# Kernel optimization log

Hardware: AMD Instinct MI355X
Metric: run time of the kernel (lower is better)

Reference implementation:

```python
import jax, jax.numpy as jnp
import numpy as np

N_FEATURES = 128
LENGTH = 10.0  # length_scale
N_NODES = 10000
N_EDGES = 200000


def mlp(x, W1, b1, W2, b2):
    # embedding.MLP(in, hidden, out): Linear -> SiLU -> Linear
    return jax.nn.silu(x @ W1 + b1) @ W2 + b2


def positional_encoding(dist, n_features, length):
    # sinusoidal encoding of scalar distances -> [E, n_features]
    ranks = jnp.arange(n_features // 2, dtype=dist.dtype)
    arg = dist[:, None] * ranks[None, :] * (np.pi / length)  # [E, F/2]
    return jnp.concatenate([jnp.sin(arg), jnp.cos(arg)], axis=-1)


def setup_inputs() -> dict:
    key = jax.random.key(0)
    N, E, F = N_NODES, N_EDGES, N_FEATURES
    ks = jax.random.split(key, 10)
    d = {}
    d["edge_index"] = jax.random.randint(ks[0], (2, E), 0, N)
    d["invariant_node_features"] = jax.random.normal(ks[1], (N, F), dtype=jnp.float32)
    d["equivariant_node_features"] = jax.random.normal(ks[2], (N, F, 3), dtype=jnp.float32)
    d["invariant_edge_features"] = jax.random.normal(ks[3], (E, F), dtype=jnp.float32)
    d["edge_dist"] = jax.random.uniform(ks[4], (E,), dtype=jnp.float32, minval=0.1, maxval=10.0)
    d["edge_dir"] = jax.random.normal(ks[5], (E, 3), dtype=jnp.float32)
    # phi: MLP(2F -> F -> 5F); w: MLP(F -> F -> 5F)
    d["phi_W1"] = jax.random.normal(ks[6], (2 * F, F), dtype=jnp.float32) / np.sqrt(2 * F)
    d["phi_b1"] = jnp.zeros((F,), jnp.float32)
    d["phi_W2"] = jax.random.normal(ks[7], (F, 5 * F), dtype=jnp.float32) / np.sqrt(F)
    d["phi_b2"] = jnp.zeros((5 * F,), jnp.float32)
    d["w_W1"] = jax.random.normal(ks[8], (F, F), dtype=jnp.float32) / np.sqrt(F)
    d["w_b1"] = jnp.zeros((F,), jnp.float32)
    d["w_W2"] = jax.random.normal(ks[9], (F, 5 * F), dtype=jnp.float32) / np.sqrt(F)
    d["w_b2"] = jnp.zeros((5 * F,), jnp.float32)
    return d


def reference(edge_index, invariant_node_features, equivariant_node_features,
              invariant_edge_features, edge_dist, edge_dir,
              phi_W1, phi_b1, phi_W2, phi_b2, w_W1, w_b1, w_W2, w_b2):
    F = N_FEATURES
    src, dst = edge_index[0], edge_index[1]
    # gather + concat edge features -> phi input [E, 2F]
    in_feat = jnp.concatenate([invariant_node_features[src], invariant_edge_features], axis=-1)
    pe = positional_encoding(edge_dist, F, LENGTH)  # [E, F]
    m = mlp(in_feat, phi_W1, phi_b1, phi_W2, phi_b2) * mlp(pe, w_W1, w_b1, w_W2, w_b2)  # [E, 5F]
    gates, cp_gates, scale_edge_dir, ds, de = jnp.split(m, 5, axis=-1)
    src_eq = equivariant_node_features[src]            # [E, F, 3]
    dst_eq = equivariant_node_features[dst]            # [E, F, 3]
    edir = edge_dir[:, None, :]                        # [E, 1, 3]
    # multiply_first_dim(w, x) == w[..., None] * x for [E,F] x [E,F,3]
    gated_features = gates[..., None] * src_eq
    scaled_edge_dir = scale_edge_dir[..., None] * edir
    cross = jnp.cross(jnp.broadcast_to(edir, dst_eq.shape), dst_eq)  # [E, F, 3]
    gated_cross = cp_gates[..., None] * cross
    dv = scaled_edge_dir + gated_features + gated_cross  # [E, F, 3]
    N = invariant_node_features.shape[0]
    dv = jax.ops.segment_sum(dv, dst, num_segments=N)   # [N, F, 3]
    ds = jax.ops.segment_sum(ds, dst, num_segments=N)   # [N, F]
    return (equivariant_node_features + dv,
            invariant_node_features + ds,
            invariant_edge_features + de)
```

## Files before the change

### kernel.cpp

```cpp
#include <hip/hip_runtime.h>
#include <math.h>

#define E_EDGES 200000
#define N_NODES 10000
#define FDIM    128

typedef __attribute__((ext_vector_type(8))) short  short8;
typedef __attribute__((ext_vector_type(4))) float  float4v;

#define WT1_OFF   0
#define WTW1_OFF  32768
#define WT2_OFF   49152
#define WTW2_OFF  131072
#define W_TOTAL   212992
#define CNT_BYTE  425984
#define CUR_BYTE  465984
#define PERM_BYTE 505984

#define EQ_OUT_SZ   (N_NODES * FDIM * 3)
#define INV_OUT_SZ  (N_NODES * FDIM)

__device__ __forceinline__ unsigned short f2bf(float x) {
    union { float f; unsigned u; } v; v.f = x;
    unsigned r = v.u + 0x7fffu + ((v.u >> 16) & 1u);
    return (unsigned short)(r >> 16);
}
__device__ __forceinline__ float bf2f(unsigned short h) {
    union { unsigned u; float f; } v; v.u = ((unsigned)h) << 16; return v.f;
}

__global__ void prep_fused(const float* __restrict__ phiW1,
                           const float* __restrict__ wW1,
                           const float* __restrict__ phiW2,
                           const float* __restrict__ wW2,
                           unsigned short* __restrict__ ws,
                           int* __restrict__ counts,
                           const float* __restrict__ eq,
                           const float* __restrict__ inv,
                           float* __restrict__ out) {
    int t = blockIdx.x * 256 + threadIdx.x;
    if (t < N_NODES) counts[t] = 0;
    if (t < W_TOTAL) {
        if (t < 32768) {
            int n = t >> 8, k = t & 255;
            ws[WT1_OFF + t] = f2bf(phiW1[k * 128 + n]);
        } else if (t < 49152) {
            int i = t - 32768; int n = i >> 7, k = i & 127;
            ws[WTW1_OFF + i] = f2bf(wW1[k * 128 + n]);
        } else if (t < 131072) {
            int i = t - 49152; int n = i >> 7, k = i & 127;
            ws[WT2_OFF + i] = f2bf(phiW2[k * 640 + n]);
        } else {
            int i = t - 131072; int n = i >> 7, k = i & 127;
            ws[WTW2_OFF + i] = f2bf(wW2[k * 640 + n]);
        }
    }
    if (t < EQ_OUT_SZ / 4) {
        ((float4v*)out)[t] = ((const float4v*)eq)[t];
    } else {
        int u = t - EQ_OUT_SZ / 4;
        ((float4v*)(out + EQ_OUT_SZ))[u] = ((const float4v*)inv)[u];
    }
}

__global__ void hist_kernel(const int* __restrict__ eidx, int* __restrict__ counts) {
    int e = blockIdx.x * 256 + threadIdx.x;
    if (e < E_EDGES) atomicAdd(&counts[eidx[E_EDGES + e]], 1);
}
__global__ __launch_bounds__(1024)
void scan_kernel(const int* __restrict__ counts, int* __restrict__ cursor) {
    __shared__ int sums[1024];
    const int t = threadIdx.x;
    const int base = t * 10;
    int local[10];
    int s = 0;
    #pragma unroll
    for (int j = 0; j < 10; ++j) {
        int b = base + j;
        int v = (b < N_NODES) ? counts[b] : 0;
        local[j] = s; s += v;
    }
    sums[t] = s;
    __syncthreads();
    for (int off = 1; off < 1024; off <<= 1) {
        int v = (t >= off) ? sums[t - off] : 0;
        __syncthreads();
        sums[t] += v;
        __syncthreads();
    }
    int pre = (t > 0) ? sums[t - 1] : 0;
    #pragma unroll
    for (int j = 0; j < 10; ++j) {
        int b = base + j;
        if (b < N_NODES) cursor[b] = pre + local[j];
    }
}
__global__ void scatter_kernel(const int* __restrict__ eidx,
                               int* __restrict__ cursor, int* __restrict__ perm) {
    int e = blockIdx.x * 256 + threadIdx.x;
    if (e < E_EDGES) {
        int d = eidx[E_EDGES + e];
        int pos = atomicAdd(&cursor[d], 1);
        perm[pos] = e;
    }
}

__global__ __launch_bounds__(256, 3)
void edge_kernel(const int*   __restrict__ eidx,
                 const float* __restrict__ node_inv,
                 const float* __restrict__ eqf,
                 const float* __restrict__ edge_inv,
                 const float* __restrict__ dist,
                 const float* __restrict__ dir,
                 const float* __restrict__ phi_b1,
                 const float* __restrict__ phi_b2,
                 const float* __restrict__ w_b1,
                 const float* __restrict__ w_b2,
                 const unsigned short* __restrict__ wsW,
                 const int* __restrict__ perm,
                 float* __restrict__ out) {
    __shared__ __align__(16) unsigned char smem_u[34816];
    __shared__ unsigned short A1b[32][136];
    __shared__ int   s_e[32], s_src[32], s_dst[32];
    __shared__ float s_dir[32][3];

    unsigned short (*A1a)[136] = (unsigned short (*)[136])smem_u;
    unsigned short (*A2)[136]  = (unsigned short (*)[136])(smem_u + 8704);
    unsigned short (*H1)[136]  = (unsigned short (*)[136])(smem_u + 17408);
    unsigned short (*H2)[136]  = (unsigned short (*)[136])(smem_u + 26112);
    float (*DVS)[65][4]        = (float (*)[65][4])smem_u;

    const int tid = threadIdx.x;
    const int p0  = blockIdx.x * 32;

    if (tid < 32) {
        int e = perm[p0 + tid];
        s_e[tid]   = e;
        s_src[tid] = eidx[e];
        s_dst[tid] = eidx[E_EDGES + e];
        s_dir[tid][0] = dir[e * 3 + 0];
        s_dir[tid][1] = dir[e * 3 + 1];
        s_dir[tid][2] = dir[e * 3 + 2];
    }
    __syncthreads();

    {
        const int i   = tid >> 3;
        const int seg = tid & 7;
        const int e   = s_e[i];
        const int k0  = seg * 32;
        const float* base = (k0 < 128)
            ? (node_inv + (size_t)s_src[i] * 128 + k0)
            : (edge_inv + (size_t)e * 128 + (k0 - 128));
        unsigned short* dst_ls = (k0 < 128) ? &A1a[i][k0] : &A1b[i][k0 - 128];
        #pragma unroll
        for (int j = 0; j < 4; ++j) {
            float4v v0 = *(const float4v*)(base + j * 8);
            float4v v1 = *(const float4v*)(base + j * 8 + 4);
            short8 sv;
            #pragma unroll
            for (int u = 0; u < 4; ++u) {
                sv[u]     = (short)f2bf(v0[u]);
                sv[u + 4] = (short)f2bf(v1[u]);
            }
            *(short8*)(dst_ls + j * 8) = sv;
        }
        const float d   = dist[e];
        const float cst = 3.14159265358979323846f / 10.0f;
        #pragma unroll
        for (int j = 0; j < 2; ++j) {
            short8 sv;
            #pragma unroll
            for (int u = 0; u < 8; ++u) {
                int f = seg * 16 + j * 8 + u;
                float val = (f < 64) ? __sinf(d * (float)f * cst)
                                     : __cosf(d * (float)(f - 64) * cst);
                sv[u] = (short)f2bf(val);
            }
            *(short8*)&A2[i][seg * 16 + j * 8] = sv;
        }
    }
    __syncthreads();

    const int wv   = tid >> 6;
    const int ln   = tid & 63;
    const int l16  = ln & 15;
    const int quad = ln >> 4;

    const unsigned short* Wt1  = wsW + WT1_OFF;
    const unsigned short* Wtw1 = wsW + WTW1_OFF;
    const unsigned short* Wt2  = wsW + WT2_OFF;
    const unsigned short* Wtw2 = wsW + WTW2_OFF;

    const float4v zero4 = {0.f, 0.f, 0.f, 0.f};

    float4v acc1[2][2], acc2[2][2];
    #pragma unroll
    for (int rt = 0; rt < 2; ++rt)
        #pragma unroll
        for (int ct = 0; ct < 2; ++ct) { acc1[rt][ct] = zero4; acc2[rt][ct] = zero4; }

    #pragma unroll
    for (int kk = 0; kk < 4; ++kk) {
        const int k = kk * 32 + quad * 8;
        short8 a0 = *(const short8*)&A1a[l16][k];
        short8 a1 = *(const short8*)&A1a[16 + l16][k];
        #pragma unroll
        for (int ct = 0; ct < 2; ++ct) {
            const int n = wv * 32 + ct * 16 + l16;
            short8 b = *(const short8*)&Wt1[n * 256 + k];
            acc1[0][ct] = __builtin_amdgcn_mfma_f32_16x16x32_bf16(a0, b, acc1[0][ct], 0, 0, 0);
            acc1[1][ct] = __builtin_amdgcn_mfma_f32_16x16x32_bf16(a1, b, acc1[1][ct], 0, 0, 0);
        }
    }
    #pragma unroll
    for (int kk = 0; kk < 4; ++kk) {
        const int k = kk * 32 + quad * 8;
        short8 a0 = *(const short8*)&A1b[l16][k];
        short8 a1 = *(const short8*)&A1b[16 + l16][k];
        #pragma unroll
        for (int ct = 0; ct < 2; ++ct) {
            const int n = wv * 32 + ct * 16 + l16;
            short8 b = *(const short8*)&Wt1[n * 256 + 128 + k];
            acc1[0][ct] = __builtin_amdgcn_mfma_f32_16x16x32_bf16(a0, b, acc1[0][ct], 0, 0, 0);
            acc1[1][ct] = __builtin_amdgcn_mfma_f32_16x16x32_bf16(a1, b, acc1[1][ct], 0, 0, 0);
        }
    }
    #pragma unroll
    for (int kk = 0; kk < 4; ++kk) {
        const int k = kk * 32 + quad * 8;
        short8 a0 = *(const short8*)&A2[l16][k];
        short8 a1 = *(const short8*)&A2[16 + l16][k];
        #pragma unroll
        for (int ct = 0; ct < 2; ++ct) {
            const int n = wv * 32 + ct * 16 + l16;
            short8 b = *(const short8*)&Wtw1[n * 128 + k];
            acc2[0][ct] = __builtin_amdgcn_mfma_f32_16x16x32_bf16(a0, b, acc2[0][ct], 0, 0, 0);
            acc2[1][ct] = __builtin_amdgcn_mfma_f32_16x16x32_bf16(a1, b, acc2[1][ct], 0, 0, 0);
        }
    }
    #pragma unroll
    for (int ct = 0; ct < 2; ++ct) {
        const int n = wv * 32 + ct * 16 + l16;
        const float b1v  = phi_b1[n];
        const float bw1v = w_b1[n];
        #pragma unroll
        for (int rt = 0; rt < 2; ++rt)
            #pragma unroll
            for (int r = 0; r < 4; ++r) {
                const int row = rt * 16 + quad * 4 + r;
                float x = acc1[rt][ct][r] + b1v;
                H1[row][n] = f2bf(x / (1.f + __expf(-x)));
                float y = acc2[rt][ct][r] + bw1v;
                H2[row][n] = f2bf(y / (1.f + __expf(-y)));
            }
    }
    __syncthreads();

    float* eq_out   = out;
    float* inv_out  = out + EQ_OUT_SZ;
    float* edge_out = out + EQ_OUT_SZ + INV_OUT_SZ;

    short8 ha[2][4], hb[2][4];
    #pragma unroll
    for (int rt = 0; rt < 2; ++rt)
        #pragma unroll
        for (int kk = 0; kk < 4; ++kk) {
            const int k = kk * 32 + quad * 8;
            ha[rt][kk] = *(const short8*)&H1[rt * 16 + l16][k];
            hb[rt][kk] = *(const short8*)&H2[rt * 16 + l16][k];
        }
    __syncthreads();

    const int red_f = tid >> 2;
    const int red_c = tid & 3;

    #pragma unroll
    for (int fc2 = 0; fc2 < 2; ++fc2) {
        float4v mv[2][5];
        #pragma unroll
        for (int g = 0; g < 5; ++g) {
            const int n = g * 128 + fc2 * 64 + wv * 16 + l16;
            float4v p1a = zero4, p1b = zero4, p2a = zero4, p2b = zero4;
            #pragma unroll
            for (int kk = 0; kk < 4; ++kk) {
                const int k = kk * 32 + quad * 8;
                short8 b1f = *(const short8*)&Wt2[n * 128 + k];
                short8 b2f = *(const short8*)&Wtw2[n * 128 + k];
                p1a = __builtin_amdgcn_mfma_f32_16x16x32_bf16(ha[0][kk], b1f, p1a, 0, 0, 0);
                p1b = __builtin_amdgcn_mfma_f32_16x16x32_bf16(ha[1][kk], b1f, p1b, 0, 0, 0);
                p2a = __builtin_amdgcn_mfma_f32_16x16x32_bf16(hb[0][kk], b2f, p2a, 0, 0, 0);
                p2b = __builtin_amdgcn_mfma_f32_16x16x32_bf16(hb[1][kk], b2f, p2b, 0, 0, 0);
            }
            const float b2v  = phi_b2[n];
            const float bw2v = w_b2[n];
            mv[0][g] = (p1a + b2v) * (p2a + bw2v);
            mv[1][g] = (p1b + b2v) * (p2b + bw2v);
        }
        {
            const int fl = wv * 16 + l16;
            const int fg = fc2 * 64 + fl;
            #pragma unroll
            for (int rt = 0; rt < 2; ++rt) {
                #pragma unroll
                for (int r = 0; r < 4; ++r) {
                    const int row = rt * 16 + quad * 4 + r;
                    const float gate = mv[rt][0][r];
                    const float cpg  = mv[rt][1][r];
                    const float sc   = mv[rt][2][r];
                    const float dsv  = mv[rt][3][r];
                    const float dev  = mv[rt][4][r];
                    const int sn = s_src[row], dn = s_dst[row], e = s_e[row];
                    const float ex = s_dir[row][0], ey = s_dir[row][1], ez = s_dir[row][2];
                    const float* se = eqf + ((size_t)sn * 128 + fg) * 3;
                    const float* dq = eqf + ((size_t)dn * 128 + fg) * 3;
                    const float sx = se[0], sy = se[1], sz = se[2];
                    const float dx = dq[0], dy = dq[1], dz = dq[2];
                    const float cx = ey * dz - ez * dy;
                    const float cy = ez * dx - ex * dz;
                    const float cz = ex * dy - ey * dx;
                    float4v v;
                    v[0] = sc * ex + gate * sx + cpg * cx;
                    v[1] = sc * ey + gate * sy + cpg * cy;
                    v[2] = sc * ez + gate * sz + cpg * cz;
                    v[3] = dsv;
                    *(float4v*)&DVS[row][fl] = v;
                    edge_out[(size_t)e * 128 + fg] = bf2f(A1b[row][fg]) + dev;
                }
            }
        }
        __syncthreads();
        {
            const int fgr = fc2 * 64 + red_f;
            float acc = 0.f;
            int prev = s_dst[0];
            #pragma unroll
            for (int r = 0; r < 32; ++r) {
                const int d = s_dst[r];
                const float v = DVS[r][red_f][red_c];
                if (d != prev) {
                    if (red_c < 3) atomicAdd(eq_out + ((size_t)prev * 128 + fgr) * 3 + red_c, acc);
                    else           atomicAdd(inv_out + (size_t)prev * 128 + fgr, acc);
                    acc = 0.f; prev = d;
                }
                acc += v;
            }
            if (red_c < 3) atomicAdd(eq_out + ((size_t)prev * 128 + fgr) * 3 + red_c, acc);
            else           atomicAdd(inv_out + (size_t)prev * 128 + fgr, acc);
        }
        __syncthreads();
    }
}

extern "C" void kernel_launch(void* const* d_in, const int* in_sizes, int n_in,
                              void* d_out, int out_size, void* d_ws, size_t ws_size,
                              hipStream_t stream) {
    const int*   eidx     = (const int*)d_in[0];
    const float* node_inv = (const float*)d_in[1];
    const float* eqf      = (const float*)d_in[2];
    const float* edge_inv = (const float*)d_in[3];
    const float* dist     = (const float*)d_in[4];
    const float* dir      = (const float*)d_in[5];
    const float* phi_W1   = (const float*)d_in[6];
    const float* phi_b1   = (const float*)d_in[7];
    const float* phi_W2   = (const float*)d_in[8];
    const float* phi_b2   = (const float*)d_in[9];
    const float* w_W1     = (const float*)d_in[10];
    const float* w_b1     = (const float*)d_in[11];
    const float* w_W2     = (const float*)d_in[12];
    const float* w_b2     = (const float*)d_in[13];
    float* out = (float*)d_out;
    unsigned short* wsW = (unsigned short*)d_ws;
    int* counts = (int*)((char*)d_ws + CNT_BYTE);
    int* cursor = (int*)((char*)d_ws + CUR_BYTE);
    int* perm   = (int*)((char*)d_ws + PERM_BYTE);

    prep_fused<<<(EQ_OUT_SZ + INV_OUT_SZ) / 4 / 256, 256, 0, stream>>>(
        phi_W1, w_W1, phi_W2, w_W2, wsW, counts, eqf, node_inv, out);
    hist_kernel<<<(E_EDGES + 255) / 256, 256, 0, stream>>>(eidx, counts);
    scan_kernel<<<1, 1024, 0, stream>>>(counts, cursor);
    scatter_kernel<<<(E_EDGES + 255) / 256, 256, 0, stream>>>(eidx, cursor, perm);
    edge_kernel<<<E_EDGES / 32, 256, 0, stream>>>(eidx, node_inv, eqf, edge_inv, dist, dir,
                                                  phi_b1, phi_b2, w_b1, w_b2, wsW, perm, out);
}
```

Before: 713.5 us.

## Compute positional encoding in registers, swizzle LDS tiles, raise occupancy, remap blocks per XCD

Removes the A2 LDS tile by computing the sinusoidal positional encoding directly into MFMA operand registers, and shrinks shared memory by replacing padded rows with an XOR-swizzled layout. Together these cut LDS per block enough that launch bounds can be raised from 3 to 4 blocks per CU. Block IDs are remapped so each XCD processes a contiguous range of sorted edges, which should improve L2 locality for destination atomics. The edge-feature bf16 values are loaded into registers before the DVS buffer overwrites that LDS region. In exchange, register pressure rises and the sin/cos work is duplicated across the waves.

```diff
diff --git a/kernel.cpp b/kernel.cpp
--- a/kernel.cpp
+++ b/kernel.cpp
@@ -27,6 +27,17 @@
 }
 __device__ __forceinline__ float bf2f(unsigned short h) {
     union { unsigned u; float f; } v; v.u = ((unsigned)h) << 16; return v.f;
+}
+
+__device__ __forceinline__ unsigned short* tile_ptr(unsigned short* base, int row, int col) {
+    unsigned off = (unsigned)(row * 256 + col * 2);
+    off ^= (unsigned)((row & 7) << 4);
+    return (unsigned short*)((char*)base + off);
+}
+__device__ __forceinline__ float* dvs_ptr(float* base, int row, int fl, int c) {
+    unsigned off = (unsigned)(row * 1024 + fl * 16 + c * 4);
+    off ^= (unsigned)((row & 7) << 4);
+    return (float*)((char*)base + off);
 }
 
 __global__ void prep_fused(const float* __restrict__ phiW1,
@@ -105,7 +116,7 @@
     }
 }
 
-__global__ __launch_bounds__(256, 3)
+__global__ __launch_bounds__(256, 4)
 void edge_kernel(const int*   __restrict__ eidx,
                  const float* __restrict__ node_inv,
                  const float* __restrict__ eqf,
@@ -119,19 +130,25 @@
                  const unsigned short* __restrict__ wsW,
                  const int* __restrict__ perm,
                  float* __restrict__ out) {
-    __shared__ __align__(16) unsigned char smem_u[34816];
-    __shared__ unsigned short A1b[32][136];
+    __shared__ __align__(16) unsigned char smem_u[32768];
     __shared__ int   s_e[32], s_src[32], s_dst[32];
     __shared__ float s_dir[32][3];
-
-    unsigned short (*A1a)[136] = (unsigned short (*)[136])smem_u;
-    unsigned short (*A2)[136]  = (unsigned short (*)[136])(smem_u + 8704);
-    unsigned short (*H1)[136]  = (unsigned short (*)[136])(smem_u + 17408);
-    unsigned short (*H2)[136]  = (unsigned short (*)[136])(smem_u + 26112);
-    float (*DVS)[65][4]        = (float (*)[65][4])smem_u;
+    __shared__ float s_dist[32];
+
+    unsigned short* A1a = (unsigned short*)smem_u;
+    unsigned short* A1b = (unsigned short*)(smem_u + 8192);
+    unsigned short* H1  = (unsigned short*)(smem_u + 16384);
+    unsigned short* H2  = (unsigned short*)(smem_u + 24576);
+    float*          DVSf = (float*)smem_u;
 
     const int tid = threadIdx.x;
-    const int p0  = blockIdx.x * 32;
+
+    const int NW = E_EDGES / 32;
+    const int q  = NW >> 3, r8 = NW & 7;
+    const int xcd = blockIdx.x & 7, idx = blockIdx.x >> 3;
+    const int swz_bid = (xcd < r8) ? (xcd * (q + 1) + idx)
+                                   : (r8 * (q + 1) + (xcd - r8) * q + idx);
+    const int p0 = swz_bid * 32;
 
     if (tid < 32) {
         int e = perm[p0 + tid];
@@ -141,18 +158,19 @@
         s_dir[tid][0] = dir[e * 3 + 0];
         s_dir[tid][1] = dir[e * 3 + 1];
         s_dir[tid][2] = dir[e * 3 + 2];
+        s_dist[tid]  = dist[e];
     }
     __syncthreads();
 
     {
         const int i   = tid >> 3;
         const int seg = tid & 7;
-        const int e   = s_e[i];
         const int k0  = seg * 32;
-        const float* base = (k0 < 128)
-            ? (node_inv + (size_t)s_src[i] * 128 + k0)
-            : (edge_inv + (size_t)e * 128 + (k0 - 128));
-        unsigned short* dst_ls = (k0 < 128) ? &A1a[i][k0] : &A1b[i][k0 - 128];
+        const float* base;
+        unsigned short* tb;
+        int c0;
+        if (k0 < 128) { base = node_inv + (size_t)s_src[i] * 128 + k0; tb = A1a; c0 = k0; }
+        else          { base = edge_inv + (size_t)s_e[i]  * 128 + (k0 - 128); tb = A1b; c0 = k0 - 128; }
         #pragma unroll
         for (int j = 0; j < 4; ++j) {
             float4v v0 = *(const float4v*)(base + j * 8);
@@ -163,21 +181,7 @@
                 sv[u]     = (short)f2bf(v0[u]);
                 sv[u + 4] = (short)f2bf(v1[u]);
             }
-            *(short8*)(dst_ls + j * 8) = sv;
-        }
-        const float d   = dist[e];
-        const float cst = 3.14159265358979323846f / 10.0f;
-        #pragma unroll
-        for (int j = 0; j < 2; ++j) {
-            short8 sv;
-            #pragma unroll
-            for (int u = 0; u < 8; ++u) {
-                int f = seg * 16 + j * 8 + u;
-                float val = (f < 64) ? __sinf(d * (float)f * cst)
-                                     : __cosf(d * (float)(f - 64) * cst);
-                sv[u] = (short)f2bf(val);
-            }
-            *(short8*)&A2[i][seg * 16 + j * 8] = sv;
+            *(short8*)tile_ptr(tb, i, c0 + j * 8) = sv;
         }
     }
     __syncthreads();
@@ -203,8 +207,8 @@
     #pragma unroll
     for (int kk = 0; kk < 4; ++kk) {
         const int k = kk * 32 + quad * 8;
-        short8 a0 = *(const short8*)&A1a[l16][k];
-        short8 a1 = *(const short8*)&A1a[16 + l16][k];
+        short8 a0 = *(const short8*)tile_ptr(A1a, l16, k);
+        short8 a1 = *(const short8*)tile_ptr(A1a, 16 + l16, k);
         #pragma unroll
         for (int ct = 0; ct < 2; ++ct) {
             const int n = wv * 32 + ct * 16 + l16;
@@ -216,8 +220,8 @@
     #pragma unroll
     for (int kk = 0; kk < 4; ++kk) {
         const int k = kk * 32 + quad * 8;
-        short8 a0 = *(const short8*)&A1b[l16][k];
-        short8 a1 = *(const short8*)&A1b[16 + l16][k];
+        short8 a0 = *(const short8*)tile_ptr(A1b, l16, k);
+        short8 a1 = *(const short8*)tile_ptr(A1b, 16 + l16, k);
         #pragma unroll
         for (int ct = 0; ct < 2; ++ct) {
             const int n = wv * 32 + ct * 16 + l16;
@@ -226,17 +230,36 @@
             acc1[1][ct] = __builtin_amdgcn_mfma_f32_16x16x32_bf16(a1, b, acc1[1][ct], 0, 0, 0);
         }
     }
-    #pragma unroll
-    for (int kk = 0; kk < 4; ++kk) {
-        const int k = kk * 32 + quad * 8;
-        short8 a0 = *(const short8*)&A2[l16][k];
-        short8 a1 = *(const short8*)&A2[16 + l16][k];
-        #pragma unroll
-        for (int ct = 0; ct < 2; ++ct) {
-            const int n = wv * 32 + ct * 16 + l16;
-            short8 b = *(const short8*)&Wtw1[n * 128 + k];
-            acc2[0][ct] = __builtin_amdgcn_mfma_f32_16x16x32_bf16(a0, b, acc2[0][ct], 0, 0, 0);
-            acc2[1][ct] = __builtin_amdgcn_mfma_f32_16x16x32_bf16(a1, b, acc2[1][ct], 0, 0, 0);
+    {
+        const float cst = 3.14159265358979323846f / 10.0f;
+        const float d0 = s_dist[l16] * cst;
+        const float d1 = s_dist[16 + l16] * cst;
+        short8 pe0[4], pe1[4];
+        #pragma unroll
+        for (int kk = 0; kk < 4; ++kk) {
+            short8 s0, s1;
+            #pragma unroll
+            for (int u = 0; u < 8; ++u) {
+                const int f = kk * 32 + quad * 8 + u;
+                const float fa = (float)((kk < 2) ? f : (f - 64));
+                float v0, v1;
+                if (kk < 2) { v0 = __sinf(d0 * fa); v1 = __sinf(d1 * fa); }
+                else        { v0 = __cosf(d0 * fa); v1 = __cosf(d1 * fa); }
+                s0[u] = (short)f2bf(v0);
+                s1[u] = (short)f2bf(v1);
+            }
+            pe0[kk] = s0; pe1[kk] = s1;
+        }
+        #pragma unroll
+        for (int kk = 0; kk < 4; ++kk) {
+            const int k = kk * 32 + quad * 8;
+            #pragma unroll
+            for (int ct = 0; ct < 2; ++ct) {
+                const int n = wv * 32 + ct * 16 + l16;
+                short8 b = *(const short8*)&Wtw1[n * 128 + k];
+                acc2[0][ct] = __builtin_amdgcn_mfma_f32_16x16x32_bf16(pe0[kk], b, acc2[0][ct], 0, 0, 0);
+                acc2[1][ct] = __builtin_amdgcn_mfma_f32_16x16x32_bf16(pe1[kk], b, acc2[1][ct], 0, 0, 0);
+            }
         }
     }
     #pragma unroll
@@ -250,9 +273,9 @@
             for (int r = 0; r < 4; ++r) {
                 const int row = rt * 16 + quad * 4 + r;
                 float x = acc1[rt][ct][r] + b1v;
-                H1[row][n] = f2bf(x / (1.f + __expf(-x)));
+                *tile_ptr(H1, row, n) = f2bf(x / (1.f + __expf(-x)));
                 float y = acc2[rt][ct][r] + bw1v;
-                H2[row][n] = f2bf(y / (1.f + __expf(-y)));
+                *tile_ptr(H2, row, n) = f2bf(y / (1.f + __expf(-y)));
             }
     }
     __syncthreads();
@@ -267,9 +290,18 @@
         #pragma unroll
         for (int kk = 0; kk < 4; ++kk) {
             const int k = kk * 32 + quad * 8;
-            ha[rt][kk] = *(const short8*)&H1[rt * 16 + l16][k];
-            hb[rt][kk] = *(const short8*)&H2[rt * 16 + l16][k];
-        }
+            ha[rt][kk] = *(const short8*)tile_ptr(H1, rt * 16 + l16, k);
+            hb[rt][kk] = *(const short8*)tile_ptr(H2, rt * 16 + l16, k);
+        }
+    unsigned short a1bv[2][8];
+    #pragma unroll
+    for (int fc2 = 0; fc2 < 2; ++fc2)
+        #pragma unroll
+        for (int rt = 0; rt < 2; ++rt)
+            #pragma unroll
+            for (int rr = 0; rr < 4; ++rr)
+                a1bv[fc2][rt * 4 + rr] =
+                    *tile_ptr(A1b, rt * 16 + quad * 4 + rr, fc2 * 64 + wv * 16 + l16);
     __syncthreads();
 
     const int red_f = tid >> 2;
@@ -324,8 +356,8 @@
                     v[1] = sc * ey + gate * sy + cpg * cy;
                     v[2] = sc * ez + gate * sz + cpg * cz;
                     v[3] = dsv;
-                    *(float4v*)&DVS[row][fl] = v;
-                    edge_out[(size_t)e * 128 + fg] = bf2f(A1b[row][fg]) + dev;
+                    *(float4v*)dvs_ptr(DVSf, row, fl, 0) = v;
+                    edge_out[(size_t)e * 128 + fg] = bf2f(a1bv[fc2][rt * 4 + r]) + dev;
                 }
             }
         }
@@ -337,7 +369,7 @@
             #pragma unroll
             for (int r = 0; r < 32; ++r) {
                 const int d = s_dst[r];
-                const float v = DVS[r][red_f][red_c];
+                const float v = *dvs_ptr(DVSf, r, red_f, red_c);
                 if (d != prev) {
                     if (red_c < 3) atomicAdd(eq_out + ((size_t)prev * 128 + fgr) * 3 + red_c, acc);
                     else           atomicAdd(inv_out + (size_t)prev * 128 + fgr, acc);
```

After: 818.9 us. 1.15x slower.
